# Optimization experiments

Hardware: AMD Instinct MI355X
Metric: run time of the kernel (lower is better)

Reference implementation:

```python
import jax, jax.numpy as jnp
import numpy as np

EPS = 1e-5

def conv1x1_bn(x, W, b, gamma, beta, mean, var):
    # x: (B,C,H,W); W: (O,C) 1x1 conv; BN in eval mode with running stats
    y = jnp.einsum('bchw,oc->bohw', x, W) + b[None, :, None, None]
    scale = gamma / jnp.sqrt(var + EPS)
    return y * scale[None, :, None, None] + (beta - mean * scale)[None, :, None, None]

def setup_inputs() -> dict:
    key = jax.random.key(0)
    ks = jax.random.split(key, 12)
    B, C, H, W = 8, 64, 128, 256
    d = {
        'fea_left': jax.random.normal(ks[0], (B, C, H, W), jnp.float32),
        'fea_right': jax.random.normal(ks[1], (B, C, H, W), jnp.float32),
        'Wq': jax.random.normal(ks[2], (C, C), jnp.float32) * (1.0 / np.sqrt(C)),
        'bq': jax.random.normal(ks[3], (C,), jnp.float32) * 0.02,
        'gq': 1.0 + 0.1 * jax.random.normal(ks[4], (C,), jnp.float32),
        'betaq': 0.02 * jax.random.normal(ks[5], (C,), jnp.float32),
        'mq': 0.02 * jax.random.normal(ks[6], (C,), jnp.float32),
        'vq': jax.random.uniform(ks[7], (C,), jnp.float32, 0.5, 1.5),
        'Wk': jax.random.normal(ks[8], (C, C), jnp.float32) * (1.0 / np.sqrt(C)),
        'bk': jax.random.normal(ks[9], (C,), jnp.float32) * 0.02,
        'gk': 1.0 + 0.1 * jax.random.normal(ks[10], (C,), jnp.float32),
        'betak': 0.02 * jax.random.normal(ks[11], (C,), jnp.float32),
        'mk': 0.02 * jax.random.normal(jax.random.fold_in(key, 100), (C,), jnp.float32),
        'vk': jax.random.uniform(jax.random.fold_in(key, 101), (C,), jnp.float32, 0.5, 1.5),
    }
    return d

def _attend(src, tgt, Wq, bq, gq, betaq, mq, vq, Wk, bk, gk, betak, mk, vk):
    # query from src, key from tgt, values are raw tgt features
    c = src.shape[1]
    Q = conv1x1_bn(src, Wq, bq, gq, betaq, mq, vq)   # (B,C,H,W)
    K = conv1x1_bn(tgt, Wk, bk, gk, betak, mk, vk)   # (B,C,H,W)
    # cost: (B,H,Wq,Wk) = Q^T K over channels, per image row
    cost = jnp.einsum('bchw,bchv->bhwv', Q, K) / c
    attn = jax.nn.softmax(cost, axis=-1)
    out = jnp.einsum('bhwv,bchv->bchw', attn, tgt)   # back to (B,C,H,W)
    return out

def reference(fea_left, fea_right, Wq, bq, gq, betaq, mq, vq, Wk, bk, gk, betak, mk, vk):
    cxr = _attend(fea_left, fea_right, Wq, bq, gq, betaq, mq, vq, Wk, bk, gk, betak, mk, vk)
    enh = _attend(fea_right, fea_left, Wq, bq, gq, betaq, mq, vq, Wk, bk, gk, betak, mk, vk)
    return (cxr, enh)
```

## Files before the change

### kernel.cpp

```cpp
#include <hip/hip_runtime.h>
#include <hip/hip_bf16.h>

#define HW_ 32768
#define OUTHALF 16777216ULL
#define SMEM_BYTES 100352

typedef short short8  __attribute__((ext_vector_type(8)));
typedef short short4v __attribute__((ext_vector_type(4)));
typedef float f32x4   __attribute__((ext_vector_type(4)));
typedef unsigned int uint4v __attribute__((ext_vector_type(4)));

__device__ __forceinline__ unsigned short f2bf(float f) {
  unsigned u = __builtin_bit_cast(unsigned, f);
  u += 0x7fffu + ((u >> 16) & 1u);
  return (unsigned short)(u >> 16);
}
__device__ __forceinline__ short f2bfn(float f) {
  __hip_bfloat16 h = __float2bfloat16(f);
  return __builtin_bit_cast(short, h);
}
__device__ __forceinline__ unsigned pkw(float lo, float hi) {
  unsigned short a = (unsigned short)f2bfn(lo), b = (unsigned short)f2bfn(hi);
  return ((unsigned)b << 16) | (unsigned)a;
}
__device__ __forceinline__ char* swz(char* base, int row, int colByte) {
  return base + row * 128 + (colByte ^ ((row & 7) << 4));
}
__device__ __forceinline__ f32x4 zero4() { f32x4 z = {0.f, 0.f, 0.f, 0.f}; return z; }

__device__ __forceinline__ void xpose(const f32x4 (&p)[4], int g,
                                      short8& f0, short8& f1) {
  unsigned W00 = pkw(p[0][0], p[0][1]), W01 = pkw(p[0][2], p[0][3]);
  unsigned W10 = pkw(p[1][0], p[1][1]), W11 = pkw(p[1][2], p[1][3]);
  unsigned W20 = pkw(p[2][0], p[2][1]), W21 = pkw(p[2][2], p[2][3]);
  unsigned W30 = pkw(p[3][0], p[3][1]), W31 = pkw(p[3][2], p[3][3]);
  const bool h2 = (g & 2) != 0;
  unsigned SA0 = h2 ? W10 : W00, SA1 = h2 ? W11 : W01;
  unsigned SA2 = h2 ? W30 : W20, SA3 = h2 ? W31 : W21;
  unsigned SB0 = h2 ? W00 : W10, SB1 = h2 ? W01 : W11;
  unsigned SB2 = h2 ? W20 : W30, SB3 = h2 ? W21 : W31;
  unsigned ra0 = __shfl_xor((int)SA0, 16), ra1 = __shfl_xor((int)SA1, 16);
  unsigned ra2 = __shfl_xor((int)SA2, 16), ra3 = __shfl_xor((int)SA3, 16);
  unsigned rb0 = __shfl_xor((int)SB0, 32), rb1 = __shfl_xor((int)SB1, 32);
  unsigned rb2 = __shfl_xor((int)SB2, 32), rb3 = __shfl_xor((int)SB3, 32);
  unsigned rc0 = __shfl_xor((int)SB0, 48), rc1 = __shfl_xor((int)SB1, 48);
  unsigned rc2 = __shfl_xor((int)SB2, 48), rc3 = __shfl_xor((int)SB3, 48);
  unsigned a0 = g==0 ? SA0 : g==1 ? rc0 : g==2 ? rb0 : ra0;
  unsigned a1 = g==0 ? SA1 : g==1 ? rc1 : g==2 ? rb1 : ra1;
  unsigned a2 = g==0 ? SA2 : g==1 ? rc2 : g==2 ? rb2 : ra2;
  unsigned a3 = g==0 ? SA3 : g==1 ? rc3 : g==2 ? rb3 : ra3;
  unsigned b0 = g==3 ? SA0 : g==2 ? rc0 : g==1 ? rb0 : ra0;
  unsigned b1 = g==3 ? SA1 : g==2 ? rc1 : g==1 ? rb1 : ra1;
  unsigned b2 = g==3 ? SA2 : g==2 ? rc2 : g==1 ? rb2 : ra2;
  unsigned b3 = g==3 ? SA3 : g==2 ? rc3 : g==1 ? rb3 : ra3;
  uint4v u0 = {a0, a1, b0, b1};
  uint4v u1 = {a2, a3, b2, b3};
  f0 = __builtin_bit_cast(short8, u0);
  f1 = __builtin_bit_cast(short8, u1);
}

__global__ void pam_setup(const float* __restrict__ Wq, const float* __restrict__ bq,
                          const float* __restrict__ gq, const float* __restrict__ betaq,
                          const float* __restrict__ mq, const float* __restrict__ vq,
                          const float* __restrict__ Wk, const float* __restrict__ gk,
                          const float* __restrict__ vk,
                          short* __restrict__ Mbt, float* __restrict__ u) {
  int blk = blockIdx.x, tid = threadIdx.x;
  if (blk < 16) {
    int entry = blk * 256 + tid;
    int y = entry >> 6, x = entry & 63;
    float acc = 0.f;
    for (int o = 0; o < 64; ++o) {
      float sq = gq[o] * rsqrtf(vq[o] + 1e-5f);
      float sk = gk[o] * rsqrtf(vk[o] + 1e-5f);
      acc += Wq[o * 64 + x] * sq * Wk[o * 64 + y] * sk;
    }
    Mbt[y * 64 + x] = (short)f2bf(acc);
  } else if (tid < 64) {
    int y = tid;
    float acc = 0.f;
    for (int o = 0; o < 64; ++o) {
      float sq = gq[o] * rsqrtf(vq[o] + 1e-5f);
      float sk = gk[o] * rsqrtf(vk[o] + 1e-5f);
      float bqq = bq[o] * sq + betaq[o] - mq[o] * sq;
      acc += bqq * Wk[o * 64 + y] * sk;
    }
    u[y] = acc;
  }
}

__global__ __launch_bounds__(1024, 4) void pam_main(
    const float* __restrict__ fl, const float* __restrict__ fr,
    const short* __restrict__ Mbt, const float* __restrict__ uvec,
    float* __restrict__ out) {
  extern __shared__ __align__(16) char sm[];
  char* XLt = sm;
  char* XRt = sm + 32768;
  char* Xn  = sm + 65536;
  float* Db = (float*)(sm + 98304);

  const int tid  = threadIdx.x;
  const int lane = tid & 63;
  const int wave = tid >> 6;
  const int l15  = lane & 15;
  const int g    = lane >> 4;
  const int bb   = blockIdx.x >> 7;
  const int hh   = blockIdx.x & 127;
  const int rowOff = hh * 256;
  const int base_b = bb * 64;
  const int at   = wave >> 3;
  const int w0   = (wave & 7) * 32;

  const int dirT = tid >> 9;
  const int vcc  = (tid >> 3) & 63;
  const int vv8  = (tid & 7) * 8;
  const float* srcv = dirT ? fl : fr;
  const float* vbase = srcv + (size_t)(base_b + vcc) * HW_ + rowOff + vv8;
  char* XnW = Xn + dirT * 16384;

  f32x4 A0 = *(const f32x4*)vbase;
  f32x4 A1 = *(const f32x4*)(vbase + 4);

  #pragma unroll
  for (int it = 0; it < 8; ++it) {
    int unit = it * 1024 + tid;
    int tensor = unit >> 12;
    int rem = unit & 4095;
    int cq = rem >> 8;
    int p  = rem & 255;
    const float* s = (tensor ? fr : fl) + (size_t)(base_b + cq * 4) * HW_ + rowOff + p;
    float v0 = s[0], v1 = s[HW_], v2 = s[2 * HW_], v3 = s[3 * HW_];
    short4v pk;
    pk[0] = f2bfn(v0); pk[1] = f2bfn(v1);
    pk[2] = f2bfn(v2); pk[3] = f2bfn(v3);
    *(short4v*)swz(tensor ? XRt : XLt, p, cq * 8) = pk;
  }
  {
    short8 pk;
    pk[0] = f2bfn(A0[0]); pk[1] = f2bfn(A0[1]);
    pk[2] = f2bfn(A0[2]); pk[3] = f2bfn(A0[3]);
    pk[4] = f2bfn(A1[0]); pk[5] = f2bfn(A1[1]);
    pk[6] = f2bfn(A1[2]); pk[7] = f2bfn(A1[3]);
    *(short8*)swz(XnW, vcc, vv8 * 2) = pk;
  }
  A0 = *(const f32x4*)(vbase + 64);
  A1 = *(const f32x4*)(vbase + 68);
  __syncthreads();

  char* Xq  = at ? XRt : XLt;
  char* Xkv = at ? XLt : XRt;

  short8 bq_[2][2];
  #pragma unroll
  for (int nj = 0; nj < 2; ++nj) {
    short8 xb0 = *(const short8*)swz(Xq, w0 + nj * 16 + l15, (8 * g) * 2);
    short8 xb1 = *(const short8*)swz(Xq, w0 + nj * 16 + l15, (32 + 8 * g) * 2);
    f32x4 qa[4];
    #pragma unroll
    for (int mi = 0; mi < 4; ++mi) {
      qa[mi] = zero4();
      short8 am0 = *(const short8*)(Mbt + (mi * 16 + l15) * 64 + 8 * g);
      short8 am1 = *(const short8*)(Mbt + (mi * 16 + l15) * 64 + 32 + 8 * g);
      qa[mi] = __builtin_amdgcn_mfma_f32_16x16x32_bf16(am0, xb0, qa[mi], 0, 0, 0);
      qa[mi] = __builtin_amdgcn_mfma_f32_16x16x32_bf16(am1, xb1, qa[mi], 0, 0, 0);
      f32x4 uv = *(const f32x4*)(uvec + mi * 16 + 4 * g);
      #pragma unroll
      for (int r = 0; r < 4; ++r) qa[mi][r] += uv[r];
    }
    xpose(qa, g, bq_[nj][0], bq_[nj][1]);
  }

  f32x4 acc_o[2][4];
  #pragma unroll
  for (int i = 0; i < 2; ++i)
    #pragma unroll
    for (int j = 0; j < 4; ++j) acc_o[i][j] = zero4();
  float dacc0 = 0.f, dacc1 = 0.f;

  #pragma unroll
  for (int vt = 0; vt < 4; ++vt) {
    if (vt < 3) {
      short8 pk;
      pk[0] = f2bfn(A0[0]); pk[1] = f2bfn(A0[1]);
      pk[2] = f2bfn(A0[2]); pk[3] = f2bfn(A0[3]);
      pk[4] = f2bfn(A1[0]); pk[5] = f2bfn(A1[1]);
      pk[6] = f2bfn(A1[2]); pk[7] = f2bfn(A1[3]);
      *(short8*)swz(XnW + ((vt + 1) & 1) * 8192, vcc, vv8 * 2) = pk;
      if (vt < 2) {
        A0 = *(const f32x4*)(vbase + (vt + 2) * 64);
        A1 = *(const f32x4*)(vbase + (vt + 2) * 64 + 4);
      }
    }
    f32x4 ps[2][4];
    #pragma unroll
    for (int mi = 0; mi < 4; ++mi) {
      short8 af0 = *(const short8*)swz(Xkv, vt * 64 + mi * 16 + l15, (8 * g) * 2);
      short8 af1 = *(const short8*)swz(Xkv, vt * 64 + mi * 16 + l15, (32 + 8 * g) * 2);
      #pragma unroll
      for (int nj = 0; nj < 2; ++nj) {
        ps[nj][mi] = zero4();
        ps[nj][mi] = __builtin_amdgcn_mfma_f32_16x16x32_bf16(af0, bq_[nj][0], ps[nj][mi], 0, 0, 0);
        ps[nj][mi] = __builtin_amdgcn_mfma_f32_16x16x32_bf16(af1, bq_[nj][1], ps[nj][mi], 0, 0, 0);
      }
    }
    short8 pf[2][2];
    #pragma unroll
    for (int nj = 0; nj < 2; ++nj) {
      float dl = 0.f;
      #pragma unroll
      for (int mi = 0; mi < 4; ++mi) {
        #pragma unroll
        for (int r = 0; r < 4; ++r)
          ps[nj][mi][r] = __expf(ps[nj][mi][r] * 0.015625f);
        dl += ps[nj][mi][0] + ps[nj][mi][1] + ps[nj][mi][2] + ps[nj][mi][3];
      }
      if (nj == 0) dacc0 += dl; else dacc1 += dl;
      xpose(ps[nj], g, pf[nj][0], pf[nj][1]);
    }
    char* XnC = Xn + at * 16384 + (vt & 1) * 8192;
    #pragma unroll
    for (int kk = 0; kk < 2; ++kk)
      #pragma unroll
      for (int nj2 = 0; nj2 < 4; ++nj2) {
        short8 xb = *(const short8*)swz(XnC, nj2 * 16 + l15, (kk * 32 + 8 * g) * 2);
        acc_o[0][nj2] = __builtin_amdgcn_mfma_f32_16x16x32_bf16(pf[0][kk], xb, acc_o[0][nj2], 0, 0, 0);
        acc_o[1][nj2] = __builtin_amdgcn_mfma_f32_16x16x32_bf16(pf[1][kk], xb, acc_o[1][nj2], 0, 0, 0);
      }
    if (vt < 3) __syncthreads();
  }

  float* outp = out + (at ? OUTHALF : 0) + (size_t)base_b * HW_ + rowOff;
  dacc0 += __shfl_xor(dacc0, 16); dacc0 += __shfl_xor(dacc0, 32);
  dacc1 += __shfl_xor(dacc1, 16); dacc1 += __shfl_xor(dacc1, 32);
  if (lane < 16) {
    Db[at * 256 + w0 + lane]      = __builtin_amdgcn_rcpf(dacc0);
    Db[at * 256 + w0 + 16 + lane] = __builtin_amdgcn_rcpf(dacc1);
  }
  #pragma unroll
  for (int nj = 0; nj < 2; ++nj) {
    f32x4 rd = *(const f32x4*)(Db + at * 256 + w0 + nj * 16 + 4 * g);
    #pragma unroll
    for (int nj2 = 0; nj2 < 4; ++nj2) {
      int c = nj2 * 16 + l15;
      f32x4 v;
      v[0] = acc_o[nj][nj2][0] * rd[0];
      v[1] = acc_o[nj][nj2][1] * rd[1];
      v[2] = acc_o[nj][nj2][2] * rd[2];
      v[3] = acc_o[nj][nj2][3] * rd[3];
      *(f32x4*)(outp + (size_t)c * HW_ + w0 + nj * 16 + 4 * g) = v;
    }
  }
}

extern "C" void kernel_launch(void* const* d_in, const int* in_sizes, int n_in,
                              void* d_out, int out_size, void* d_ws, size_t ws_size,
                              hipStream_t stream) {
  (void)in_sizes; (void)n_in; (void)out_size; (void)ws_size;
  const float* fl    = (const float*)d_in[0];
  const float* fr    = (const float*)d_in[1];
  const float* Wq    = (const float*)d_in[2];
  const float* bq    = (const float*)d_in[3];
  const float* gq    = (const float*)d_in[4];
  const float* betaq = (const float*)d_in[5];
  const float* mq    = (const float*)d_in[6];
  const float* vq    = (const float*)d_in[7];
  const float* Wk    = (const float*)d_in[8];
  const float* gk    = (const float*)d_in[10];
  const float* vk    = (const float*)d_in[13];
  short* Mbt = (short*)d_ws;
  float* u   = (float*)((char*)d_ws + 8192);
  float* out = (float*)d_out;

  hipFuncSetAttribute((const void*)pam_main,
                      hipFuncAttributeMaxDynamicSharedMemorySize, SMEM_BYTES);
  pam_setup<<<17, 256, 0, stream>>>(Wq, bq, gq, betaq, mq, vq, Wk, gk, vk, Mbt, u);
  pam_main<<<1024, 1024, SMEM_BYTES, stream>>>(fl, fr, Mbt, u, out);
}
```

Measured before the change: 126.4 us.

## Split attention directions across workgroups and feed PV MFMA directly from score registers

Each workgroup now handles one direction for one image row (2048 workgroups of 512 threads instead of 1024 of 1024), with an XCD-aware block remap. Both K and Q/V tiles are still loaded per block, so the transposed feature staging is duplicated across the two blocks of a row. The P·V product switches to the 16x16x16 bf16 MFMA so exp'd scores feed it straight from the accumulator layout, removing the cross-lane transpose shuffles. The V tile uses a new swizzle, and the softmax denominator is broadcast with shuffles instead of LDS. LDS per block shrinks, which may raise occupancy, at the cost of redundant global loads and more, smaller MFMAs.

```diff
diff --git a/kernel.cpp b/kernel.cpp
--- a/kernel.cpp
+++ b/kernel.cpp
@@ -3,11 +3,12 @@
 
 #define HW_ 32768
 #define OUTHALF 16777216ULL
-#define SMEM_BYTES 100352
+#define SMEM_BYTES 81920
 
 typedef short short8  __attribute__((ext_vector_type(8)));
 typedef short short4v __attribute__((ext_vector_type(4)));
 typedef float f32x4   __attribute__((ext_vector_type(4)));
+typedef unsigned int uint2v __attribute__((ext_vector_type(2)));
 typedef unsigned int uint4v __attribute__((ext_vector_type(4)));
 
 __device__ __forceinline__ unsigned short f2bf(float f) {
@@ -25,6 +26,9 @@
 }
 __device__ __forceinline__ char* swz(char* base, int row, int colByte) {
   return base + row * 128 + (colByte ^ ((row & 7) << 4));
+}
+__device__ __forceinline__ char* swzV(char* base, int row, int colByte) {
+  return base + row * 128 + (colByte ^ ((row & 3) << 5));
 }
 __device__ __forceinline__ f32x4 zero4() { f32x4 z = {0.f, 0.f, 0.f, 0.f}; return z; }
 
@@ -89,7 +93,7 @@
   }
 }
 
-__global__ __launch_bounds__(1024, 4) void pam_main(
+__global__ __launch_bounds__(512, 4) void pam_main(
     const float* __restrict__ fl, const float* __restrict__ fr,
     const short* __restrict__ Mbt, const float* __restrict__ uvec,
     float* __restrict__ out) {
@@ -97,33 +101,32 @@
   char* XLt = sm;
   char* XRt = sm + 32768;
   char* Xn  = sm + 65536;
-  float* Db = (float*)(sm + 98304);
 
   const int tid  = threadIdx.x;
   const int lane = tid & 63;
   const int wave = tid >> 6;
   const int l15  = lane & 15;
   const int g    = lane >> 4;
-  const int bb   = blockIdx.x >> 7;
-  const int hh   = blockIdx.x & 127;
+  const int wg = ((blockIdx.x & 7) << 8) | (blockIdx.x >> 3);
+  const int bh = wg >> 1;
+  const int at = wg & 1;
+  const int bb = bh >> 7;
+  const int hh = bh & 127;
   const int rowOff = hh * 256;
   const int base_b = bb * 64;
-  const int at   = wave >> 3;
-  const int w0   = (wave & 7) * 32;
-
-  const int dirT = tid >> 9;
-  const int vcc  = (tid >> 3) & 63;
-  const int vv8  = (tid & 7) * 8;
-  const float* srcv = dirT ? fl : fr;
-  const float* vbase = srcv + (size_t)(base_b + vcc) * HW_ + rowOff + vv8;
-  char* XnW = Xn + dirT * 16384;
+  const int w0   = wave * 32;
+
+  const int vc = tid >> 3;
+  const int v8 = (tid & 7) * 8;
+  const float* srcv = at ? fl : fr;
+  const float* vbase = srcv + (size_t)(base_b + vc) * HW_ + rowOff + v8;
 
   f32x4 A0 = *(const f32x4*)vbase;
   f32x4 A1 = *(const f32x4*)(vbase + 4);
 
   #pragma unroll
-  for (int it = 0; it < 8; ++it) {
-    int unit = it * 1024 + tid;
+  for (int it = 0; it < 16; ++it) {
+    int unit = it * 512 + tid;
     int tensor = unit >> 12;
     int rem = unit & 4095;
     int cq = rem >> 8;
@@ -141,7 +144,7 @@
     pk[2] = f2bfn(A0[2]); pk[3] = f2bfn(A0[3]);
     pk[4] = f2bfn(A1[0]); pk[5] = f2bfn(A1[1]);
     pk[6] = f2bfn(A1[2]); pk[7] = f2bfn(A1[3]);
-    *(short8*)swz(XnW, vcc, vv8 * 2) = pk;
+    *(short8*)swzV(Xn, vc, v8 * 2) = pk;
   }
   A0 = *(const f32x4*)(vbase + 64);
   A1 = *(const f32x4*)(vbase + 68);
@@ -185,60 +188,56 @@
       pk[2] = f2bfn(A0[2]); pk[3] = f2bfn(A0[3]);
       pk[4] = f2bfn(A1[0]); pk[5] = f2bfn(A1[1]);
       pk[6] = f2bfn(A1[2]); pk[7] = f2bfn(A1[3]);
-      *(short8*)swz(XnW + ((vt + 1) & 1) * 8192, vcc, vv8 * 2) = pk;
+      *(short8*)swzV(Xn + ((vt + 1) & 1) * 8192, vc, v8 * 2) = pk;
       if (vt < 2) {
         A0 = *(const f32x4*)(vbase + (vt + 2) * 64);
         A1 = *(const f32x4*)(vbase + (vt + 2) * 64 + 4);
       }
     }
-    f32x4 ps[2][4];
+    char* XnB = Xn + (vt & 1) * 8192;
+
     #pragma unroll
     for (int mi = 0; mi < 4; ++mi) {
       short8 af0 = *(const short8*)swz(Xkv, vt * 64 + mi * 16 + l15, (8 * g) * 2);
       short8 af1 = *(const short8*)swz(Xkv, vt * 64 + mi * 16 + l15, (32 + 8 * g) * 2);
+      short4v bv[4];
+      #pragma unroll
+      for (int nj2 = 0; nj2 < 4; ++nj2)
+        bv[nj2] = *(const short4v*)swzV(XnB, nj2 * 16 + l15, (mi * 16 + 4 * g) * 2);
       #pragma unroll
       for (int nj = 0; nj < 2; ++nj) {
-        ps[nj][mi] = zero4();
-        ps[nj][mi] = __builtin_amdgcn_mfma_f32_16x16x32_bf16(af0, bq_[nj][0], ps[nj][mi], 0, 0, 0);
-        ps[nj][mi] = __builtin_amdgcn_mfma_f32_16x16x32_bf16(af1, bq_[nj][1], ps[nj][mi], 0, 0, 0);
-      }
-    }
-    short8 pf[2][2];
-    #pragma unroll
-    for (int nj = 0; nj < 2; ++nj) {
-      float dl = 0.f;
-      #pragma unroll
-      for (int mi = 0; mi < 4; ++mi) {
+        f32x4 ps = zero4();
+        ps = __builtin_amdgcn_mfma_f32_16x16x32_bf16(af0, bq_[nj][0], ps, 0, 0, 0);
+        ps = __builtin_amdgcn_mfma_f32_16x16x32_bf16(af1, bq_[nj][1], ps, 0, 0, 0);
         #pragma unroll
         for (int r = 0; r < 4; ++r)
-          ps[nj][mi][r] = __expf(ps[nj][mi][r] * 0.015625f);
-        dl += ps[nj][mi][0] + ps[nj][mi][1] + ps[nj][mi][2] + ps[nj][mi][3];
+          ps[r] = __expf(ps[r] * 0.015625f);
+        if (nj == 0) dacc0 += ps[0] + ps[1] + ps[2] + ps[3];
+        else         dacc1 += ps[0] + ps[1] + ps[2] + ps[3];
+        uint2v pw;
+        pw[0] = pkw(ps[0], ps[1]);
+        pw[1] = pkw(ps[2], ps[3]);
+        short4v pa = __builtin_bit_cast(short4v, pw);
+        #pragma unroll
+        for (int nj2 = 0; nj2 < 4; ++nj2)
+          acc_o[nj][nj2] = __builtin_amdgcn_mfma_f32_16x16x16bf16_1k(
+              pa, bv[nj2], acc_o[nj][nj2], 0, 0, 0);
       }
-      if (nj == 0) dacc0 += dl; else dacc1 += dl;
-      xpose(ps[nj], g, pf[nj][0], pf[nj][1]);
-    }
-    char* XnC = Xn + at * 16384 + (vt & 1) * 8192;
-    #pragma unroll
-    for (int kk = 0; kk < 2; ++kk)
-      #pragma unroll
-      for (int nj2 = 0; nj2 < 4; ++nj2) {
-        short8 xb = *(const short8*)swz(XnC, nj2 * 16 + l15, (kk * 32 + 8 * g) * 2);
-        acc_o[0][nj2] = __builtin_amdgcn_mfma_f32_16x16x32_bf16(pf[0][kk], xb, acc_o[0][nj2], 0, 0, 0);
-        acc_o[1][nj2] = __builtin_amdgcn_mfma_f32_16x16x32_bf16(pf[1][kk], xb, acc_o[1][nj2], 0, 0, 0);
-      }
+    }
     if (vt < 3) __syncthreads();
   }
 
-  float* outp = out + (at ? OUTHALF : 0) + (size_t)base_b * HW_ + rowOff;
   dacc0 += __shfl_xor(dacc0, 16); dacc0 += __shfl_xor(dacc0, 32);
   dacc1 += __shfl_xor(dacc1, 16); dacc1 += __shfl_xor(dacc1, 32);
-  if (lane < 16) {
-    Db[at * 256 + w0 + lane]      = __builtin_amdgcn_rcpf(dacc0);
-    Db[at * 256 + w0 + 16 + lane] = __builtin_amdgcn_rcpf(dacc1);
-  }
+  float dinv0 = __builtin_amdgcn_rcpf(dacc0);
+  float dinv1 = __builtin_amdgcn_rcpf(dacc1);
+  float* outp = out + (at ? OUTHALF : 0) + (size_t)base_b * HW_ + rowOff;
   #pragma unroll
   for (int nj = 0; nj < 2; ++nj) {
-    f32x4 rd = *(const f32x4*)(Db + at * 256 + w0 + nj * 16 + 4 * g);
+    f32x4 rd;
+    #pragma unroll
+    for (int r = 0; r < 4; ++r)
+      rd[r] = __shfl(nj ? dinv1 : dinv0, 4 * g + r);
     #pragma unroll
     for (int nj2 = 0; nj2 < 4; ++nj2) {
       int c = nj2 * 16 + l15;
@@ -274,5 +273,5 @@
   hipFuncSetAttribute((const void*)pam_main,
                       hipFuncAttributeMaxDynamicSharedMemorySize, SMEM_BYTES);
   pam_setup<<<17, 256, 0, stream>>>(Wq, bq, gq, betaq, mq, vq, Wk, gk, vk, Mbt, u);
-  pam_main<<<1024, 1024, SMEM_BYTES, stream>>>(fl, fr, Mbt, u, out);
-}
+  pam_main<<<2048, 512, SMEM_BYTES, stream>>>(fl, fr, Mbt, u, out);
+}
```

After: 248.6 us. 1.97x slower.
